# Kernel tuning notes

Measured on AMD Instinct MI355X. Metric: run time of the kernel, lower is better.

Reference implementation:

```python
import jax, jax.numpy as jnp
import numpy as np

NUM_DST = 100_000   # blk.num_dst()
E = 1_000_000       # number of temporal edges
U_N = 200_000       # unique node rows
U_E = 100_000       # unique edge-feature rows
U_T = 100_000       # unique time deltas
DN, DE, DT, DOUT, H = 172, 172, 100, 100, 2
NEG_SLOPE = 0.2
LN_EPS = 1e-5


def _lin_init(k, fan_in, fan_out):
    return jax.random.normal(k, (fan_in, fan_out), jnp.float32) / np.float32(np.sqrt(fan_in))


def setup_inputs() -> dict:
    key = jax.random.key(0)
    ks = jax.random.split(key, 16)
    return {
        "nodeData": jax.random.normal(ks[0], (U_N, DN), jnp.float32),
        "efeat_unique": jax.random.normal(ks[1], (U_E, DE), jnp.float32),
        "unique_time_delta": jax.random.uniform(ks[2], (U_T,), jnp.float32) * 1000.0,
        "reverse_nids": jax.random.randint(ks[3], (NUM_DST + E,), 0, U_N, jnp.int32),
        "reverse_eids": jax.random.randint(ks[4], (E,), 0, U_E, jnp.int32),
        "reverse_time_delta": jax.random.randint(ks[5], (E,), 0, U_T, jnp.int32),
        "dstindex": jax.random.randint(ks[6], (E,), 0, NUM_DST, jnp.int32),
        "num_dst": NUM_DST,
        "time_w": jax.random.normal(ks[7], (DT,), jnp.float32),
        "time_b": jax.random.normal(ks[8], (DT,), jnp.float32),
        "Wqn": _lin_init(ks[9], DN, DOUT), "bqn": jnp.zeros((DOUT,), jnp.float32),
        "Wqt": _lin_init(ks[10], DT, DOUT), "bqt": jnp.zeros((DOUT,), jnp.float32),
        "Wkvn": _lin_init(ks[11], DN, 2 * DOUT), "bkvn": jnp.zeros((2 * DOUT,), jnp.float32),
        "Wkve": _lin_init(ks[12], DE, 2 * DOUT), "bkve": jnp.zeros((2 * DOUT,), jnp.float32),
        "Wkvt": _lin_init(ks[13], DT, 2 * DOUT), "bkvt": jnp.zeros((2 * DOUT,), jnp.float32),
        "Wout": _lin_init(ks[14], DN + DOUT, DOUT), "bout": jnp.zeros((DOUT,), jnp.float32),
        "ln_g": jnp.ones((DOUT,), jnp.float32), "ln_b": jnp.zeros((DOUT,), jnp.float32),
    }


def _forward(nodeData, efeat_unique, unique_time_delta, time_w, time_b,
             Wqn, bqn, Wqt, bqt, Wkvn, bkvn, Wkve, bkve, Wkvt, bkvt,
             Wout, bout, ln_g, ln_b,
             reverse_nids, reverse_eids, reverse_time_delta, dstindex, num_dst):
    node_dst_inv = reverse_nids[:num_dst]   # dst -> unique node row
    node_inv = reverse_nids[num_dst:]       # edge -> unique node row (src/nbr)
    # TimeEncode: cos(t * w + b); t=0 for all dst nodes (single shared row).
    nbrs_time_feat = jnp.cos(unique_time_delta[:, None] * time_w[None, :] + time_b[None, :])  # [U_T, DT]
    time_dst = jnp.cos(time_b)[None, :]                                                       # [1, DT]
    # Queries: project unique tables once, then gather (dedup trick).
    q = (nodeData @ Wqn + bqn)[node_dst_inv] + (time_dst @ Wqt + bqt)  # [num_dst, DOUT]
    Q = q[dstindex]                                                    # [E, DOUT]
    # Keys/values: fused node+edge+time projections, gathered per edge.
    Z = ((nodeData @ Wkvn + bkvn)[node_inv]
         + (efeat_unique @ Wkve + bkve)[reverse_eids]
         + (nbrs_time_feat @ Wkvt + bkvt)[reverse_time_delta])         # [E, 2*DOUT]
    dh = DOUT // H
    K = Z[:, :DOUT].reshape(-1, H, dh)
    V = Z[:, DOUT:].reshape(-1, H, dh)
    Qh = Q.reshape(-1, H, dh)
    attn = jax.nn.leaky_relu(jnp.sum(Qh * K, axis=2), NEG_SLOPE)       # [E, H]
    # edge softmax over incoming edges of each dst node
    m = jax.lax.stop_gradient(jax.ops.segment_max(attn, dstindex, num_segments=num_dst))
    e = jnp.exp(attn - m[dstindex])
    s = jax.ops.segment_sum(e, dstindex, num_segments=num_dst)
    a = e / s[dstindex]                                                # [E, H]
    # edge reduce (sum) -> [num_dst, DOUT]
    out = jax.ops.segment_sum((V * a[:, :, None]).reshape(-1, DOUT), dstindex, num_segments=num_dst)
    out = jnp.concatenate([out, nodeData[node_dst_inv]], axis=1)       # [num_dst, DOUT+DN]
    out = jax.nn.relu(out @ Wout + bout)
    mu = out.mean(axis=-1, keepdims=True)
    var = out.var(axis=-1, keepdims=True)
    return (out - mu) / jnp.sqrt(var + LN_EPS) * ln_g + ln_b


def reference(nodeData, efeat_unique, unique_time_delta, reverse_nids, reverse_eids,
              reverse_time_delta, dstindex, num_dst, time_w, time_b,
              Wqn, bqn, Wqt, bqt, Wkvn, bkvn, Wkve, bkve, Wkvt, bkvt,
              Wout, bout, ln_g, ln_b):
    return _forward(nodeData, efeat_unique, unique_time_delta, time_w, time_b,
                    Wqn, bqn, Wqt, bqt, Wkvn, bkvn, Wkve, bkve, Wkvt, bkvt,
                    Wout, bout, ln_g, ln_b,
                    reverse_nids, reverse_eids, reverse_time_delta, dstindex, num_dst)
```

## Files before the change

### kernel.cpp

```cpp
#include <hip/hip_runtime.h>
#include <hip/hip_bf16.h>

typedef __hip_bfloat16 bf16;

#define K_NUM_DST 100000
#define K_E       1000000
#define K_UN      200000
#define K_UE      100000
#define K_UT      100000
#define K_DN      172
#define K_DT      100
#define K_DOUT    100
#define K_DKV     200
#define K_DCAT    272
#define K_NEG_SLOPE 0.2f
#define K_LN_EPS    1e-5f

__device__ __forceinline__ float bits2f(unsigned short u){
  union { float f; unsigned int i; } c; c.i = ((unsigned int)u) << 16; return c.f;
}
__device__ __forceinline__ float t2f(float v){ return v; }
__device__ __forceinline__ float t2f(bf16 v){ return __bfloat162float(v); }

template<typename TIN> struct OutStore;
template<> struct OutStore<float>{
  static __device__ __forceinline__ void st(void* o, size_t i, float v){ ((float*)o)[i] = v; }
};
template<> struct OutStore<bf16>{
  static __device__ __forceinline__ void st(void* o, size_t i, float v){ ((bf16*)o)[i] = __float2bfloat16(v); }
};

template<typename TIN> struct Ld4;
template<> struct Ld4<float>{
  static __device__ __forceinline__ float4 ld(const void* base, size_t eo){
    return *(const float4*)((const float*)base + eo);
  }
};
template<> struct Ld4<bf16>{
  static __device__ __forceinline__ float4 ld(const void* base, size_t eo){
    ushort4 u = *(const ushort4*)((const unsigned short*)base + eo);
    float4 f; f.x = bits2f(u.x); f.y = bits2f(u.y); f.z = bits2f(u.z); f.w = bits2f(u.w);
    return f;
  }
};

template<typename TAB> __device__ __forceinline__ void store4(TAB* p, float a, float b, float c, float d);
template<> __device__ __forceinline__ void store4<float>(float* p, float a, float b, float c, float d){
  float4 v; v.x=a; v.y=b; v.z=c; v.w=d; *(float4*)p = v;
}
template<> __device__ __forceinline__ void store4<bf16>(bf16* p, float a, float b, float c, float d){
  p[0]=__float2bfloat16(a); p[1]=__float2bfloat16(b); p[2]=__float2bfloat16(c); p[3]=__float2bfloat16(d);
}

__global__ void detect_kernel(const unsigned short* __restrict__ nd, int* __restrict__ dflag){
  unsigned int i = blockIdx.x * 256u + threadIdx.x;
  unsigned short u = nd[i];
  if (((u >> 7) & 0xFF) == 0xFF) atomicOr(dflag, 1);
}

template<typename TIN>
__global__ void qt_kernel(const int* __restrict__ dflag, int want,
                          const void* time_b_v, const void* Wqt_v,
                          const void* bqt_v, float* __restrict__ qt){
  if (*dflag != want) return;
  const TIN* time_b = (const TIN*)time_b_v;
  const TIN* Wqt = (const TIN*)Wqt_v;
  const TIN* bqt = (const TIN*)bqt_v;
  int c = threadIdx.x;
  if (c >= K_DOUT) return;
  float acc = t2f(bqt[c]);
  for (int k = 0; k < K_DT; k++)
    acc += cosf(t2f(time_b[k])) * t2f(Wqt[k * K_DOUT + c]);
  qt[c] = acc;
}

template<typename TAB, typename TIN>
__global__ __launch_bounds__(320)
void node_proj_kernel(const int* __restrict__ dflag, int want,
    const void* nodeData_v, const void* Wqn_v, const void* bqn_v,
    const void* Wkvn_v, const void* bkvn_v,
    TAB* __restrict__ qn_tab, TAB* __restrict__ kvn_tab){
  if (*dflag != want) return;
  __shared__ float xs[32][68];
  int row0 = blockIdx.x * 32;
  int tid = threadIdx.x;
  int ci = tid % 75, ri = tid / 75;
  const void* W; const TIN* B; int ldw, c0;
  if (ci < 25){ W = Wqn_v;  B = (const TIN*)bqn_v;  ldw = K_DOUT; c0 = 4*ci; }
  else        { W = Wkvn_v; B = (const TIN*)bkvn_v; ldw = K_DKV;  c0 = 4*(ci-25); }
  float acc[8][4] = {};
  #pragma unroll
  for (int c = 0; c < 3; c++){
    const int ng = (c < 2) ? 16 : 11;
    if (c > 0) __syncthreads();
    for (int idx = tid; idx < 32 * ng; idx += 320){
      int r = idx / ng, g = idx % ng;
      float4 v = Ld4<TIN>::ld(nodeData_v, (size_t)(row0 + r) * K_DN + (16*c + g) * 4);
      *(float4*)&xs[r][g * 4] = v;
    }
    __syncthreads();
    if (tid < 300){
      const float* xbase = &xs[8*ri][0];
      #pragma unroll 2
      for (int g = 0; g < ng; g++){
        int kg = (16*c + g) * 4;
        float4 w0 = Ld4<TIN>::ld(W, (size_t)(kg+0) * ldw + c0);
        float4 w1 = Ld4<TIN>::ld(W, (size_t)(kg+1) * ldw + c0);
        float4 w2 = Ld4<TIN>::ld(W, (size_t)(kg+2) * ldw + c0);
        float4 w3 = Ld4<TIN>::ld(W, (size_t)(kg+3) * ldw + c0);
        #pragma unroll
        for (int i = 0; i < 8; i++){
          float4 a = *(const float4*)(xbase + i * 68 + 4*g);
          acc[i][0] = fmaf(a.x,w0.x, fmaf(a.y,w1.x, fmaf(a.z,w2.x, fmaf(a.w,w3.x, acc[i][0]))));
          acc[i][1] = fmaf(a.x,w0.y, fmaf(a.y,w1.y, fmaf(a.z,w2.y, fmaf(a.w,w3.y, acc[i][1]))));
          acc[i][2] = fmaf(a.x,w0.z, fmaf(a.y,w1.z, fmaf(a.z,w2.z, fmaf(a.w,w3.z, acc[i][2]))));
          acc[i][3] = fmaf(a.x,w0.w, fmaf(a.y,w1.w, fmaf(a.z,w2.w, fmaf(a.w,w3.w, acc[i][3]))));
        }
      }
    }
  }
  if (tid >= 300) return;
  float b0 = t2f(B[c0+0]), b1 = t2f(B[c0+1]), b2 = t2f(B[c0+2]), b3 = t2f(B[c0+3]);
  TAB* tab = (ci < 25) ? qn_tab : kvn_tab;
  #pragma unroll
  for (int i = 0; i < 8; i++){
    size_t row = row0 + 8*ri + i;
    store4<TAB>(&tab[row * ldw + c0], acc[i][0]+b0, acc[i][1]+b1, acc[i][2]+b2, acc[i][3]+b3);
  }
}

template<typename TAB, typename TIN>
__global__ __launch_bounds__(256)
void feat_proj_kernel(const int* __restrict__ dflag, int want,
    const void* A_v, const void* W_v, const void* bias_v,
    TAB* __restrict__ out_tab){
  if (*dflag != want) return;
  __shared__ float xs[40][68];
  int row0 = blockIdx.x * 40;
  int tid = threadIdx.x;
  int ci = tid % 50, ri = tid / 50;
  int c0 = 4 * ci;
  float acc[8][4] = {};
  #pragma unroll
  for (int c = 0; c < 3; c++){
    const int ng = (c < 2) ? 16 : 11;
    if (c > 0) __syncthreads();
    for (int idx = tid; idx < 40 * ng; idx += 256){
      int r = idx / ng, g = idx % ng;
      float4 v = Ld4<TIN>::ld(A_v, (size_t)(row0 + r) * K_DN + (16*c + g) * 4);
      *(float4*)&xs[r][g * 4] = v;
    }
    __syncthreads();
    if (tid < 250){
      const float* xbase = &xs[8*ri][0];
      #pragma unroll 2
      for (int g = 0; g < ng; g++){
        int kg = (16*c + g) * 4;
        float4 w0 = Ld4<TIN>::ld(W_v, (size_t)(kg+0) * K_DKV + c0);
        float4 w1 = Ld4<TIN>::ld(W_v, (size_t)(kg+1) * K_DKV + c0);
        float4 w2 = Ld4<TIN>::ld(W_v, (size_t)(kg+2) * K_DKV + c0);
        float4 w3 = Ld4<TIN>::ld(W_v, (size_t)(kg+3) * K_DKV + c0);
        #pragma unroll
        for (int i = 0; i < 8; i++){
          float4 a = *(const float4*)(xbase + i * 68 + 4*g);
          acc[i][0] = fmaf(a.x,w0.x, fmaf(a.y,w1.x, fmaf(a.z,w2.x, fmaf(a.w,w3.x, acc[i][0]))));
          acc[i][1] = fmaf(a.x,w0.y, fmaf(a.y,w1.y, fmaf(a.z,w2.y, fmaf(a.w,w3.y, acc[i][1]))));
          acc[i][2] = fmaf(a.x,w0.z, fmaf(a.y,w1.z, fmaf(a.z,w2.z, fmaf(a.w,w3.z, acc[i][2]))));
          acc[i][3] = fmaf(a.x,w0.w, fmaf(a.y,w1.w, fmaf(a.z,w2.w, fmaf(a.w,w3.w, acc[i][3]))));
        }
      }
    }
  }
  if (tid >= 250) return;
  const TIN* B = (const TIN*)bias_v;
  float b0 = t2f(B[c0+0]), b1 = t2f(B[c0+1]), b2 = t2f(B[c0+2]), b3 = t2f(B[c0+3]);
  #pragma unroll
  for (int i = 0; i < 8; i++){
    size_t row = row0 + 8*ri + i;
    store4<TAB>(&out_tab[row * K_DKV + c0], acc[i][0]+b0, acc[i][1]+b1, acc[i][2]+b2, acc[i][3]+b3);
  }
}

template<typename TAB, typename TIN>
__global__ __launch_bounds__(256)
void time_proj_kernel(const int* __restrict__ dflag, int want,
    const void* utd_v, const void* time_w_v, const void* time_b_v,
    const void* Wkvt_v, const void* bkvt_v,
    TAB* __restrict__ kvt_tab){
  if (*dflag != want) return;
  __shared__ float xs[40][68];
  __shared__ float ts[40];
  int row0 = blockIdx.x * 40;
  int tid = threadIdx.x;
  if (tid < 40) ts[tid] = t2f(((const TIN*)utd_v)[row0 + tid]);
  __syncthreads();
  int ci = tid % 50, ri = tid / 50;
  int c0 = 4 * ci;
  float acc[8][4] = {};
  #pragma unroll
  for (int c = 0; c < 2; c++){
    const int ng = (c < 1) ? 16 : 9;
    const int nk = ng * 4;
    if (c > 0) __syncthreads();
    for (int idx = tid; idx < 40 * nk; idx += 256){
      int r = idx / nk, kloc = idx % nk;
      int k = 64*c + kloc;
      xs[r][kloc] = cosf(ts[r] * t2f(((const TIN*)time_w_v)[k]) + t2f(((const TIN*)time_b_v)[k]));
    }
    __syncthreads();
    if (tid < 250){
      const float* xbase = &xs[8*ri][0];
      #pragma unroll 2
      for (int g = 0; g < ng; g++){
        int kg = 64*c + 4*g;
        float4 w0 = Ld4<TIN>::ld(Wkvt_v, (size_t)(kg+0) * K_DKV + c0);
        float4 w1 = Ld4<TIN>::ld(Wkvt_v, (size_t)(kg+1) * K_DKV + c0);
        float4 w2 = Ld4<TIN>::ld(Wkvt_v, (size_t)(kg+2) * K_DKV + c0);
        float4 w3 = Ld4<TIN>::ld(Wkvt_v, (size_t)(kg+3) * K_DKV + c0);
        #pragma unroll
        for (int i = 0; i < 8; i++){
          float4 a = *(const float4*)(xbase + i * 68 + 4*g);
          acc[i][0] = fmaf(a.x,w0.x, fmaf(a.y,w1.x, fmaf(a.z,w2.x, fmaf(a.w,w3.x, acc[i][0]))));
          acc[i][1] = fmaf(a.x,w0.y, fmaf(a.y,w1.y, fmaf(a.z,w2.y, fmaf(a.w,w3.y, acc[i][1]))));
          acc[i][2] = fmaf(a.x,w0.z, fmaf(a.y,w1.z, fmaf(a.z,w2.z, fmaf(a.w,w3.z, acc[i][2]))));
          acc[i][3] = fmaf(a.x,w0.w, fmaf(a.y,w1.w, fmaf(a.z,w2.w, fmaf(a.w,w3.w, acc[i][3]))));
        }
      }
    }
  }
  if (tid >= 250) return;
  const TIN* B = (const TIN*)bkvt_v;
  float b0 = t2f(B[c0+0]), b1 = t2f(B[c0+1]), b2 = t2f(B[c0+2]), b3 = t2f(B[c0+3]);
  #pragma unroll
  for (int i = 0; i < 8; i++){
    size_t row = row0 + 8*ri + i;
    store4<TAB>(&kvt_tab[row * K_DKV + c0], acc[i][0]+b0, acc[i][1]+b1, acc[i][2]+b2, acc[i][3]+b3);
  }
}

__global__ void hist_kernel(const int* __restrict__ dstindex, int* __restrict__ counts){
  int e = blockIdx.x * blockDim.x + threadIdx.x;
  if (e < K_E) atomicAdd(&counts[dstindex[e]], 1);
}

__global__ void scan1_kernel(const int* __restrict__ counts, int* __restrict__ offsets,
                             int* __restrict__ bsum, int n){
  __shared__ int sd[256];
  int b = blockIdx.x, t = threadIdx.x;
  int base = b * 1024 + t * 4;
  int v0=0,v1=0,v2=0,v3=0;
  if (base+0 < n) v0 = counts[base+0];
  if (base+1 < n) v1 = counts[base+1];
  if (base+2 < n) v2 = counts[base+2];
  if (base+3 < n) v3 = counts[base+3];
  int s = v0+v1+v2+v3;
  sd[t] = s;
  __syncthreads();
  for (int off = 1; off < 256; off <<= 1){
    int tmp = (t >= off) ? sd[t-off] : 0;
    __syncthreads();
    sd[t] += tmp;
    __syncthreads();
  }
  int excl = sd[t] - s;
  if (base+0 < n) offsets[base+0] = excl;
  if (base+1 < n) offsets[base+1] = excl + v0;
  if (base+2 < n) offsets[base+2] = excl + v0 + v1;
  if (base+3 < n) offsets[base+3] = excl + v0 + v1 + v2;
  if (t == 255) bsum[b] = sd[255];
}

__global__ void scan2_kernel(int* bsum, int nb){
  if (threadIdx.x == 0 && blockIdx.x == 0){
    int run = 0;
    for (int i = 0; i < nb; i++){ int v = bsum[i]; bsum[i] = run; run += v; }
  }
}

__global__ void scan3_kernel(int* __restrict__ offsets, const int* __restrict__ bsum, int n){
  int i = blockIdx.x * blockDim.x + threadIdx.x;
  if (i < n) offsets[i] += bsum[i >> 10];
}

__global__ void scatter_kernel(const int* __restrict__ dstindex, const int* __restrict__ offsets,
                               int* __restrict__ cursor, int* __restrict__ edge_ids){
  int e = blockIdx.x * blockDim.x + threadIdx.x;
  if (e < K_E){
    int d = dstindex[e];
    int p = atomicAdd(&cursor[d], 1);
    edge_ids[offsets[d] + p] = e;
  }
}

template<typename TAB>
__global__ __launch_bounds__(256)
void attn_kernel(
    const int* __restrict__ reverse_nids, const int* __restrict__ reverse_eids,
    const int* __restrict__ reverse_tids,
    const int* __restrict__ dstoff, const int* __restrict__ dstcnt,
    const int* __restrict__ edge_ids,
    const TAB* __restrict__ qn_tab, const TAB* __restrict__ kvn_tab,
    const TAB* __restrict__ kve_tab, const TAB* __restrict__ kvt_tab,
    const float* __restrict__ qt, float* __restrict__ out_agg){
  int tid = threadIdx.x;
  int wave = tid >> 6;
  int l = tid & 63;
  int h = l >> 5;
  int li = l & 31;
  int dst = blockIdx.x * 4 + wave;
  int start = dstoff[dst];
  int cnt = dstcnt[dst];
  int cntw = (cnt + 1 - h) >> 1;
  bool act = (li < 25);
  int d4 = 4 * li;
  bool c0h0 = (d4+0) < 50, c1h0 = (d4+1) < 50, c2h0 = (d4+2) < 50, c3h0 = (d4+3) < 50;

  int gn = reverse_nids[dst];
  float4 q = make_float4(0.f,0.f,0.f,0.f);
  if (act){
    float4 qn = Ld4<TAB>::ld(qn_tab, (size_t)gn * K_DOUT + d4);
    float4 qtv = *(const float4*)(qt + d4);
    q.x = qn.x + qtv.x; q.y = qn.y + qtv.y; q.z = qn.z + qtv.z; q.w = qn.w + qtv.w;
  }

  float m0 = -3.0e38f, m1 = -3.0e38f, s0 = 0.f, s1 = 0.f;
  float ax = 0.f, ay = 0.f, az = 0.f, aw = 0.f;

  for (int j = 0; j < cntw; j++){
    int e   = edge_ids[start + 2*j + h];
    int nid = reverse_nids[K_NUM_DST + e];
    int eid = reverse_eids[e];
    int tde = reverse_tids[e];
    float4 kx = make_float4(0.f,0.f,0.f,0.f);
    if (act){
      float4 k1 = Ld4<TAB>::ld(kvn_tab, (size_t)nid * K_DKV + d4);
      float4 k2 = Ld4<TAB>::ld(kve_tab, (size_t)eid * K_DKV + d4);
      float4 k3 = Ld4<TAB>::ld(kvt_tab, (size_t)tde * K_DKV + d4);
      kx.x = k1.x+k2.x+k3.x; kx.y = k1.y+k2.y+k3.y; kx.z = k1.z+k2.z+k3.z; kx.w = k1.w+k2.w+k3.w;
    }
    float px = q.x*kx.x, py = q.y*kx.y, pz = q.z*kx.z, pw = q.w*kx.w;
    float p0 = (c0h0?px:0.f) + (c1h0?py:0.f) + (c2h0?pz:0.f) + (c3h0?pw:0.f);
    float p1 = (px+py+pz+pw) - p0;
    #pragma unroll
    for (int off = 16; off; off >>= 1){
      p0 += __shfl_xor(p0, off);
      p1 += __shfl_xor(p1, off);
    }
    float a0 = (p0 > 0.f) ? p0 : K_NEG_SLOPE * p0;
    float a1 = (p1 > 0.f) ? p1 : K_NEG_SLOPE * p1;
    float nm0 = fmaxf(m0, a0), nm1 = fmaxf(m1, a1);
    float al0 = __expf(m0 - nm0), al1 = __expf(m1 - nm1);
    float e0  = __expf(a0 - nm0), e1  = __expf(a1 - nm1);
    s0 = s0 * al0 + e0; s1 = s1 * al1 + e1;
    m0 = nm0; m1 = nm1;
    float4 vx = make_float4(0.f,0.f,0.f,0.f);
    if (act){
      float4 v1 = Ld4<TAB>::ld(kvn_tab, (size_t)nid * K_DKV + K_DOUT + d4);
      float4 v2 = Ld4<TAB>::ld(kve_tab, (size_t)eid * K_DKV + K_DOUT + d4);
      float4 v3 = Ld4<TAB>::ld(kvt_tab, (size_t)tde * K_DKV + K_DOUT + d4);
      vx.x = v1.x+v2.x+v3.x; vx.y = v1.y+v2.y+v3.y; vx.z = v1.z+v2.z+v3.z; vx.w = v1.w+v2.w+v3.w;
    }
    ax = ax * (c0h0?al0:al1) + (c0h0?e0:e1) * vx.x;
    ay = ay * (c1h0?al0:al1) + (c1h0?e0:e1) * vx.y;
    az = az * (c2h0?al0:al1) + (c2h0?e0:e1) * vx.z;
    aw = aw * (c3h0?al0:al1) + (c3h0?e0:e1) * vx.w;
  }

  float mo0 = __shfl_xor(m0, 32), so0 = __shfl_xor(s0, 32);
  float mo1 = __shfl_xor(m1, 32), so1 = __shfl_xor(s1, 32);
  float aox = __shfl_xor(ax, 32), aoy = __shfl_xor(ay, 32);
  float aoz = __shfl_xor(az, 32), aow = __shfl_xor(aw, 32);
  float M0 = fmaxf(m0, mo0), M1 = fmaxf(m1, mo1);
  float cs0 = __expf(m0 - M0), co0 = __expf(mo0 - M0);
  float cs1 = __expf(m1 - M1), co1 = __expf(mo1 - M1);
  float S0 = s0 * cs0 + so0 * co0;
  float S1 = s1 * cs1 + so1 * co1;
  float inv0 = (S0 > 0.f) ? 1.f / S0 : 0.f;
  float inv1 = (S1 > 0.f) ? 1.f / S1 : 0.f;
  float rx = c0h0 ? (ax*cs0 + aox*co0)*inv0 : (ax*cs1 + aox*co1)*inv1;
  float ry = c1h0 ? (ay*cs0 + aoy*co0)*inv0 : (ay*cs1 + aoy*co1)*inv1;
  float rz = c2h0 ? (az*cs0 + aoz*co0)*inv0 : (az*cs1 + aoz*co1)*inv1;
  float rw = c3h0 ? (aw*cs0 + aow*co0)*inv0 : (aw*cs1 + aow*co1)*inv1;
  if (h == 0 && act){
    float4 r; r.x=rx; r.y=ry; r.z=rz; r.w=rw;
    *(float4*)(out_agg + (size_t)dst * K_DOUT + d4) = r;
  }
}

template<typename TIN>
__global__ __launch_bounds__(256)
void final_kernel(const int* __restrict__ dflag, int want,
    const float* __restrict__ out_agg,
    const void* nodeData_v, const int* __restrict__ reverse_nids,
    const void* Wout_v, const void* bout_v,
    const void* ln_g_v, const void* ln_b_v,
    void* out){
  if (*dflag != want) return;
  __shared__ float xs[32][72];
  __shared__ float part[32][25][2];
  __shared__ float stats[32][2];
  __shared__ int gnid[32];
  int dbase = blockIdx.x * 32;
  int tid = threadIdx.x;
  if (tid < 32) gnid[tid] = reverse_nids[dbase + tid];
  __syncthreads();
  int ci = tid % 25, ri = tid / 25;
  int c0 = 4 * ci;
  float acc[4][4] = {};
  #pragma unroll
  for (int c = 0; c < 4; c++){
    if (c > 0) __syncthreads();
    for (int idx = tid; idx < 32 * 17; idx += 256){
      int r = idx / 17, g = idx % 17;
      int gk = (c * 17 + g) * 4;
      float4 v;
      if (gk < 100) v = *(const float4*)(out_agg + (size_t)(dbase + r) * K_DOUT + gk);
      else          v = Ld4<TIN>::ld(nodeData_v, (size_t)gnid[r] * K_DN + (gk - 100));
      *(float4*)&xs[r][g * 4] = v;
    }
    __syncthreads();
    if (tid < 200){
      const float* xbase = &xs[4 * ri][0];
      #pragma unroll 2
      for (int g = 0; g < 17; g++){
        int kg = (c * 17 + g) * 4;
        float4 w0 = Ld4<TIN>::ld(Wout_v, (size_t)(kg+0) * K_DOUT + c0);
        float4 w1 = Ld4<TIN>::ld(Wout_v, (size_t)(kg+1) * K_DOUT + c0);
        float4 w2 = Ld4<TIN>::ld(Wout_v, (size_t)(kg+2) * K_DOUT + c0);
        float4 w3 = Ld4<TIN>::ld(Wout_v, (size_t)(kg+3) * K_DOUT + c0);
        #pragma unroll
        for (int i = 0; i < 4; i++){
          float4 a = *(const float4*)(xbase + i * 72 + 4*g);
          acc[i][0] = fmaf(a.x,w0.x, fmaf(a.y,w1.x, fmaf(a.z,w2.x, fmaf(a.w,w3.x, acc[i][0]))));
          acc[i][1] = fmaf(a.x,w0.y, fmaf(a.y,w1.y, fmaf(a.z,w2.y, fmaf(a.w,w3.y, acc[i][1]))));
          acc[i][2] = fmaf(a.x,w0.z, fmaf(a.y,w1.z, fmaf(a.z,w2.z, fmaf(a.w,w3.z, acc[i][2]))));
          acc[i][3] = fmaf(a.x,w0.w, fmaf(a.y,w1.w, fmaf(a.z,w2.w, fmaf(a.w,w3.w, acc[i][3]))));
        }
      }
    }
  }
  if (tid < 200){
    const TIN* B = (const TIN*)bout_v;
    float b0 = t2f(B[c0+0]), b1 = t2f(B[c0+1]), b2 = t2f(B[c0+2]), b3 = t2f(B[c0+3]);
    #pragma unroll
    for (int i = 0; i < 4; i++){
      acc[i][0] = fmaxf(acc[i][0]+b0, 0.f);
      acc[i][1] = fmaxf(acc[i][1]+b1, 0.f);
      acc[i][2] = fmaxf(acc[i][2]+b2, 0.f);
      acc[i][3] = fmaxf(acc[i][3]+b3, 0.f);
      float s1 = acc[i][0]+acc[i][1]+acc[i][2]+acc[i][3];
      float s2 = acc[i][0]*acc[i][0]+acc[i][1]*acc[i][1]+acc[i][2]*acc[i][2]+acc[i][3]*acc[i][3];
      part[4*ri + i][ci][0] = s1;
      part[4*ri + i][ci][1] = s2;
    }
  }
  __syncthreads();
  if (tid < 32){
    float s1 = 0.f, s2 = 0.f;
    for (int j = 0; j < 25; j++){ s1 += part[tid][j][0]; s2 += part[tid][j][1]; }
    stats[tid][0] = s1; stats[tid][1] = s2;
  }
  __syncthreads();
  if (tid < 200){
    const TIN* G = (const TIN*)ln_g_v; const TIN* Bb = (const TIN*)ln_b_v;
    float g0 = t2f(G[c0+0]), g1 = t2f(G[c0+1]), g2 = t2f(G[c0+2]), g3 = t2f(G[c0+3]);
    float lb0 = t2f(Bb[c0+0]), lb1 = t2f(Bb[c0+1]), lb2 = t2f(Bb[c0+2]), lb3 = t2f(Bb[c0+3]);
    #pragma unroll
    for (int i = 0; i < 4; i++){
      int r = 4*ri + i;
      float mu = stats[r][0] * (1.f / K_DOUT);
      float var = stats[r][1] * (1.f / K_DOUT) - mu * mu;
      float rs = rsqrtf(var + K_LN_EPS);
      size_t o = (size_t)(dbase + r) * K_DOUT + c0;
      OutStore<TIN>::st(out, o+0, (acc[i][0]-mu)*rs*g0 + lb0);
      OutStore<TIN>::st(out, o+1, (acc[i][1]-mu)*rs*g1 + lb1);
      OutStore<TIN>::st(out, o+2, (acc[i][2]-mu)*rs*g2 + lb2);
      OutStore<TIN>::st(out, o+3, (acc[i][3]-mu)*rs*g3 + lb3);
    }
  }
}

static inline size_t al256(size_t b){ return (b + 255) & ~(size_t)255; }

template<typename TAB>
static void run_pipeline(void* const* d_in, void* out, char* ws, hipStream_t stream){
  const void* nodeData = d_in[0];
  const void* efeat    = d_in[1];
  const void* utd      = d_in[2];
  const int* reverse_nids = (const int*)d_in[3];
  const int* reverse_eids = (const int*)d_in[4];
  const int* reverse_tids = (const int*)d_in[5];
  const int* dstindex     = (const int*)d_in[6];
  const void* time_w = d_in[8];
  const void* time_b = d_in[9];
  const void* Wqn  = d_in[10]; const void* bqn  = d_in[11];
  const void* Wqt  = d_in[12]; const void* bqt  = d_in[13];
  const void* Wkvn = d_in[14]; const void* bkvn = d_in[15];
  const void* Wkve = d_in[16]; const void* bkve = d_in[17];
  const void* Wkvt = d_in[18]; const void* bkvt = d_in[19];
  const void* Wout = d_in[20]; const void* bout = d_in[21];
  const void* ln_g = d_in[22]; const void* ln_b = d_in[23];

  char* p = ws;
  int* dflag = (int*)p;       p += 256;
  TAB* qn_tab  = (TAB*)p; p += al256(sizeof(TAB) * (size_t)K_UN * K_DOUT);
  TAB* kvn_tab = (TAB*)p; p += al256(sizeof(TAB) * (size_t)K_UN * K_DKV);
  TAB* kve_tab = (TAB*)p; p += al256(sizeof(TAB) * (size_t)K_UE * K_DKV);
  TAB* kvt_tab = (TAB*)p; p += al256(sizeof(TAB) * (size_t)K_UT * K_DKV);
  float* out_agg = (float*)p; p += al256(sizeof(float) * (size_t)K_NUM_DST * K_DOUT);
  float* qt = (float*)p;      p += al256(sizeof(float) * K_DOUT);
  int* counts = (int*)p;      p += al256(sizeof(int) * K_NUM_DST);
  int* offsets = (int*)p;     p += al256(sizeof(int) * K_NUM_DST);
  int* cursor = (int*)p;      p += al256(sizeof(int) * K_NUM_DST);
  int* bsum = (int*)p;        p += al256(sizeof(int) * 512);
  int* edge_ids = (int*)p;    p += al256(sizeof(int) * (size_t)K_E);

  hipMemsetAsync(dflag, 0, 256, stream);
  hipMemsetAsync(counts, 0, sizeof(int) * K_NUM_DST, stream);
  hipMemsetAsync(cursor, 0, sizeof(int) * K_NUM_DST, stream);

  detect_kernel<<<512, 256, 0, stream>>>((const unsigned short*)nodeData, dflag);

  qt_kernel<float><<<1, 128, 0, stream>>>(dflag, 1, time_b, Wqt, bqt, qt);
  node_proj_kernel<TAB, float><<<K_UN / 32, 320, 0, stream>>>(dflag, 1, nodeData, Wqn, bqn, Wkvn, bkvn, qn_tab, kvn_tab);
  feat_proj_kernel<TAB, float><<<K_UE / 40, 256, 0, stream>>>(dflag, 1, efeat, Wkve, bkve, kve_tab);
  time_proj_kernel<TAB, float><<<K_UT / 40, 256, 0, stream>>>(dflag, 1, utd, time_w, time_b, Wkvt, bkvt, kvt_tab);
  qt_kernel<bf16><<<1, 128, 0, stream>>>(dflag, 0, time_b, Wqt, bqt, qt);
  node_proj_kernel<TAB, bf16><<<K_UN / 32, 320, 0, stream>>>(dflag, 0, nodeData, Wqn, bqn, Wkvn, bkvn, qn_tab, kvn_tab);
  feat_proj_kernel<TAB, bf16><<<K_UE / 40, 256, 0, stream>>>(dflag, 0, efeat, Wkve, bkve, kve_tab);
  time_proj_kernel<TAB, bf16><<<K_UT / 40, 256, 0, stream>>>(dflag, 0, utd, time_w, time_b, Wkvt, bkvt, kvt_tab);

  hist_kernel<<<(K_E + 255) / 256, 256, 0, stream>>>(dstindex, counts);
  int nb = (K_NUM_DST + 1023) / 1024;
  scan1_kernel<<<nb, 256, 0, stream>>>(counts, offsets, bsum, K_NUM_DST);
  scan2_kernel<<<1, 1, 0, stream>>>(bsum, nb);
  scan3_kernel<<<(K_NUM_DST + 255) / 256, 256, 0, stream>>>(offsets, bsum, K_NUM_DST);
  scatter_kernel<<<(K_E + 255) / 256, 256, 0, stream>>>(dstindex, offsets, cursor, edge_ids);

  attn_kernel<TAB><<<K_NUM_DST / 4, 256, 0, stream>>>(reverse_nids, reverse_eids, reverse_tids,
      offsets, counts, edge_ids, qn_tab, kvn_tab, kve_tab, kvt_tab, qt, out_agg);

  final_kernel<float><<<K_NUM_DST / 32, 256, 0, stream>>>(dflag, 1, out_agg, nodeData, reverse_nids,
      Wout, bout, ln_g, ln_b, out);
  final_kernel<bf16><<<K_NUM_DST / 32, 256, 0, stream>>>(dflag, 0, out_agg, nodeData, reverse_nids,
      Wout, bout, ln_g, ln_b, out);
}

extern "C" void kernel_launch(void* const* d_in, const int* in_sizes, int n_in,
                              void* d_out, int out_size, void* d_ws, size_t ws_size,
                              hipStream_t stream){
  (void)in_sizes; (void)n_in; (void)out_size;

  size_t fixed = 256 + al256(4ull * K_NUM_DST * K_DOUT) + al256(4 * K_DOUT)
               + 3 * al256(4 * K_NUM_DST) + al256(4 * 512) + al256(4ull * K_E);
  size_t tab_elems = (size_t)K_UN * K_DOUT + (size_t)K_UN * K_DKV
                   + (size_t)K_UE * K_DKV + (size_t)K_UT * K_DKV;
  size_t need_f32  = fixed + tab_elems * 4 + 8192;
  size_t need_bf16 = fixed + tab_elems * 2 + 8192;

  if (ws_size >= need_f32){
    run_pipeline<float>(d_in, d_out, (char*)d_ws, stream);
  } else if (ws_size >= need_bf16){
    run_pipeline<bf16>(d_in, d_out, (char*)d_ws, stream);
  }
}
```

Baseline: 1.738 ms.

## Use bf16 MFMA matrix cores for node, edge and time projection GEMMs

For bf16 inputs, the node, edge-feature and time projections move from scalar FMA kernels to MFMA 16x16x32 bf16 kernels. Small pre-pass kernels pack the weights into an MFMA-friendly fragment layout, and the time encoding is computed into shared memory before the matmul. The aim is to cut projection compute time. The cost is extra launches, extra workspace, and bf16 rounding of the cos time features.

```diff
diff --git a/kernel.cpp b/kernel.cpp
--- a/kernel.cpp
+++ b/kernel.cpp
@@ -2,6 +2,9 @@
 #include <hip/hip_bf16.h>
 
 typedef __hip_bfloat16 bf16;
+typedef unsigned short u16;
+typedef __attribute__((ext_vector_type(8))) short bf16x8s;
+typedef __attribute__((ext_vector_type(4))) float f32x4;
 
 #define K_NUM_DST 100000
 #define K_E       1000000
@@ -16,8 +19,21 @@
 #define K_NEG_SLOPE 0.2f
 #define K_LN_EPS    1e-5f
 
-__device__ __forceinline__ float bits2f(unsigned short u){
+#define NT_NODE 19
+#define NS_NODE 6
+#define NT_KV   13
+#define NS_KVE  6
+#define NS_KVT  4
+
+__device__ __forceinline__ float bits2f(u16 u){
   union { float f; unsigned int i; } c; c.i = ((unsigned int)u) << 16; return c.f;
+}
+__device__ __forceinline__ u16 f2bfbits(float f){
+  bf16 h = __float2bfloat16(f);
+  return *(u16*)&h;
+}
+__device__ __forceinline__ unsigned int pk2(float a, float b){
+  return (unsigned int)f2bfbits(a) | ((unsigned int)f2bfbits(b) << 16);
 }
 __device__ __forceinline__ float t2f(float v){ return v; }
 __device__ __forceinline__ float t2f(bf16 v){ return __bfloat162float(v); }
@@ -38,7 +54,7 @@
 };
 template<> struct Ld4<bf16>{
   static __device__ __forceinline__ float4 ld(const void* base, size_t eo){
-    ushort4 u = *(const ushort4*)((const unsigned short*)base + eo);
+    ushort4 u = *(const ushort4*)((const u16*)base + eo);
     float4 f; f.x = bits2f(u.x); f.y = bits2f(u.y); f.z = bits2f(u.z); f.w = bits2f(u.w);
     return f;
   }
@@ -52,9 +68,9 @@
   p[0]=__float2bfloat16(a); p[1]=__float2bfloat16(b); p[2]=__float2bfloat16(c); p[3]=__float2bfloat16(d);
 }
 
-__global__ void detect_kernel(const unsigned short* __restrict__ nd, int* __restrict__ dflag){
+__global__ void detect_kernel(const u16* __restrict__ nd, int* __restrict__ dflag){
   unsigned int i = blockIdx.x * 256u + threadIdx.x;
-  unsigned short u = nd[i];
+  u16 u = nd[i];
   if (((u >> 7) & 0xFF) == 0xFF) atomicOr(dflag, 1);
 }
 
@@ -72,6 +88,166 @@
   for (int k = 0; k < K_DT; k++)
     acc += cosf(t2f(time_b[k])) * t2f(Wqt[k * K_DOUT + c]);
   qt[c] = acc;
+}
+
+
+__global__ void pack_node_w_kernel(const int* __restrict__ dflag,
+    const u16* __restrict__ Wqn, const u16* __restrict__ Wkvn, u16* __restrict__ Bp){
+  if (*dflag != 0) return;
+  int t = blockIdx.x * 256 + threadIdx.x;
+  if (t >= NT_NODE * NS_NODE * 64) return;
+  int lane = t & 63; int cs = t >> 6; int s = cs % NS_NODE, c = cs / NS_NODE;
+  int col = c * 16 + (lane & 15);
+  int k0 = s * 32 + (lane >> 4) * 8;
+  u16 v[8];
+  #pragma unroll
+  for (int e = 0; e < 8; e++){
+    int k = k0 + e; u16 x = 0;
+    if (k < K_DN){
+      if (col < K_DOUT) x = Wqn[(size_t)k * K_DOUT + col];
+      else if (col < K_DOUT + K_DKV) x = Wkvn[(size_t)k * K_DKV + (col - K_DOUT)];
+    }
+    v[e] = x;
+  }
+  uint4 o;
+  o.x = (unsigned)v[0] | ((unsigned)v[1] << 16);
+  o.y = (unsigned)v[2] | ((unsigned)v[3] << 16);
+  o.z = (unsigned)v[4] | ((unsigned)v[5] << 16);
+  o.w = (unsigned)v[6] | ((unsigned)v[7] << 16);
+  *(uint4*)&Bp[(size_t)t * 8] = o;
+}
+
+__global__ void pack_w_kernel(const int* __restrict__ dflag,
+    const u16* __restrict__ W, int K, int N, int NT, int NS, u16* __restrict__ Bp){
+  if (*dflag != 0) return;
+  int t = blockIdx.x * 256 + threadIdx.x;
+  if (t >= NT * NS * 64) return;
+  int lane = t & 63; int cs = t >> 6; int s = cs % NS, c = cs / NS;
+  int col = c * 16 + (lane & 15);
+  int k0 = s * 32 + (lane >> 4) * 8;
+  u16 v[8];
+  #pragma unroll
+  for (int e = 0; e < 8; e++){
+    int k = k0 + e;
+    v[e] = (k < K && col < N) ? W[(size_t)k * N + col] : (u16)0;
+  }
+  uint4 o;
+  o.x = (unsigned)v[0] | ((unsigned)v[1] << 16);
+  o.y = (unsigned)v[2] | ((unsigned)v[3] << 16);
+  o.z = (unsigned)v[4] | ((unsigned)v[5] << 16);
+  o.w = (unsigned)v[6] | ((unsigned)v[7] << 16);
+  *(uint4*)&Bp[(size_t)t * 8] = o;
+}
+
+template<typename TAB>
+__global__ __launch_bounds__(256)
+void mfma_proj_kernel(const int* __restrict__ dflag,
+    const u16* __restrict__ A, int M,
+    const u16* __restrict__ Bp, int NT,
+    const u16* __restrict__ bias1, const u16* __restrict__ bias2,
+    TAB* __restrict__ out1, int N1, TAB* __restrict__ out2, int N2){
+  if (*dflag != 0) return;
+  __shared__ u16 xs[64][200];
+  int row0 = blockIdx.x * 64;
+  int tid = threadIdx.x;
+  const unsigned int* A32 = (const unsigned int*)A;
+  unsigned int* xs32 = (unsigned int*)&xs[0][0];
+  for (int j = tid; j < 64 * 86; j += 256){
+    int r = j / 86, k2 = j % 86;
+    unsigned int v = (row0 + r < M) ? A32[(size_t)(row0 + r) * 86 + k2] : 0u;
+    xs32[r * 100 + k2] = v;
+  }
+  for (int j = tid; j < 64 * 14; j += 256){
+    int r = j / 14, k2 = 86 + (j % 14);
+    xs32[r * 100 + k2] = 0u;
+  }
+  __syncthreads();
+  int lane = tid & 63, w = tid >> 6;
+  int ar = 16 * w + (lane & 15);
+  int kg = lane >> 4;
+  bf16x8s a[6];
+  #pragma unroll
+  for (int s = 0; s < 6; s++)
+    a[s] = *(const bf16x8s*)&xs[ar][s * 32 + kg * 8];
+  int co_l = lane & 15;
+  int rb = row0 + 16 * w + 4 * kg;
+  for (int c = 0; c < NT; c++){
+    const u16* bp = Bp + (size_t)(c * 6) * 512 + (size_t)lane * 8;
+    f32x4 acc = {0.f, 0.f, 0.f, 0.f};
+    #pragma unroll
+    for (int s = 0; s < 6; s++){
+      bf16x8s b = *(const bf16x8s*)(bp + s * 512);
+      acc = __builtin_amdgcn_mfma_f32_16x16x32_bf16(a[s], b, acc, 0, 0, 0);
+    }
+    int co = c * 16 + co_l;
+    float bv; TAB* op; size_t stride; int cc;
+    if (co < N1){ bv = bits2f(bias1[co]); op = out1; stride = N1; cc = co; }
+    else if (co < N1 + N2){ bv = bits2f(bias2[co - N1]); op = out2; stride = N2; cc = co - N1; }
+    else continue;
+    #pragma unroll
+    for (int r = 0; r < 4; r++){
+      int row = rb + r;
+      if (row < M) OutStore<TAB>::st(op, (size_t)row * stride + cc, acc[r] + bv);
+    }
+  }
+}
+
+template<typename TAB>
+__global__ __launch_bounds__(256)
+void mfma_time_proj_kernel(const int* __restrict__ dflag,
+    const u16* __restrict__ utd, int M,
+    const u16* __restrict__ Bp,
+    const u16* __restrict__ tw, const u16* __restrict__ tb,
+    const u16* __restrict__ bias, TAB* __restrict__ out1){
+  if (*dflag != 0) return;
+  __shared__ u16 xs[64][136];
+  __shared__ float ts[64];
+  int row0 = blockIdx.x * 64;
+  int tid = threadIdx.x;
+  if (tid < 64){
+    int r = row0 + tid;
+    ts[tid] = bits2f(utd[(r < M) ? r : (M - 1)]);
+  }
+  __syncthreads();
+  unsigned int* xs32 = (unsigned int*)&xs[0][0];
+  for (int j = tid; j < 64 * 68; j += 256){
+    int r = j / 68, k2 = j % 68;
+    int k = k2 * 2;
+    unsigned int v = 0u;
+    if (k < K_DT){
+      float c0 = cosf(ts[r] * bits2f(tw[k])     + bits2f(tb[k]));
+      float c1 = cosf(ts[r] * bits2f(tw[k + 1]) + bits2f(tb[k + 1]));
+      v = pk2(c0, c1);
+    }
+    xs32[r * 68 + k2] = v;
+  }
+  __syncthreads();
+  int lane = tid & 63, w = tid >> 6;
+  int ar = 16 * w + (lane & 15);
+  int kg = lane >> 4;
+  bf16x8s a[4];
+  #pragma unroll
+  for (int s = 0; s < 4; s++)
+    a[s] = *(const bf16x8s*)&xs[ar][s * 32 + kg * 8];
+  int co_l = lane & 15;
+  int rb = row0 + 16 * w + 4 * kg;
+  for (int c = 0; c < NT_KV; c++){
+    const u16* bp = Bp + (size_t)(c * 4) * 512 + (size_t)lane * 8;
+    f32x4 acc = {0.f, 0.f, 0.f, 0.f};
+    #pragma unroll
+    for (int s = 0; s < 4; s++){
+      bf16x8s b = *(const bf16x8s*)(bp + s * 512);
+      acc = __builtin_amdgcn_mfma_f32_16x16x32_bf16(a[s], b, acc, 0, 0, 0);
+    }
+    int co = c * 16 + co_l;
+    if (co >= K_DKV) continue;
+    float bv = bits2f(bias[co]);
+    #pragma unroll
+    for (int r = 0; r < 4; r++){
+      int row = rb + r;
+      if (row < M) OutStore<TAB>::st(out1, (size_t)row * K_DKV + co, acc[r] + bv);
+    }
+  }
 }
 
 template<typename TAB, typename TIN>
@@ -482,6 +658,10 @@
 
 static inline size_t al256(size_t b){ return (b + 255) & ~(size_t)255; }
 
+#define BP_NODE_U16 ((size_t)NT_NODE * NS_NODE * 64 * 8)
+#define BP_KVE_U16  ((size_t)NT_KV * NS_KVE * 64 * 8)
+#define BP_KVT_U16  ((size_t)NT_KV * NS_KVT * 64 * 8)
+
 template<typename TAB>
 static void run_pipeline(void* const* d_in, void* out, char* ws, hipStream_t stream){
   const void* nodeData = d_in[0];
@@ -514,21 +694,37 @@
   int* cursor = (int*)p;      p += al256(sizeof(int) * K_NUM_DST);
   int* bsum = (int*)p;        p += al256(sizeof(int) * 512);
   int* edge_ids = (int*)p;    p += al256(sizeof(int) * (size_t)K_E);
+  u16* bp_node = (u16*)p;     p += al256(2 * BP_NODE_U16);
+  u16* bp_kve  = (u16*)p;     p += al256(2 * BP_KVE_U16);
+  u16* bp_kvt  = (u16*)p;     p += al256(2 * BP_KVT_U16);
 
   hipMemsetAsync(dflag, 0, 256, stream);
   hipMemsetAsync(counts, 0, sizeof(int) * K_NUM_DST, stream);
   hipMemsetAsync(cursor, 0, sizeof(int) * K_NUM_DST, stream);
 
-  detect_kernel<<<512, 256, 0, stream>>>((const unsigned short*)nodeData, dflag);
+  detect_kernel<<<512, 256, 0, stream>>>((const u16*)nodeData, dflag);
 
   qt_kernel<float><<<1, 128, 0, stream>>>(dflag, 1, time_b, Wqt, bqt, qt);
   node_proj_kernel<TAB, float><<<K_UN / 32, 320, 0, stream>>>(dflag, 1, nodeData, Wqn, bqn, Wkvn, bkvn, qn_tab, kvn_tab);
   feat_proj_kernel<TAB, float><<<K_UE / 40, 256, 0, stream>>>(dflag, 1, efeat, Wkve, bkve, kve_tab);
   time_proj_kernel<TAB, float><<<K_UT / 40, 256, 0, stream>>>(dflag, 1, utd, time_w, time_b, Wkvt, bkvt, kvt_tab);
+
   qt_kernel<bf16><<<1, 128, 0, stream>>>(dflag, 0, time_b, Wqt, bqt, qt);
-  node_proj_kernel<TAB, bf16><<<K_UN / 32, 320, 0, stream>>>(dflag, 0, nodeData, Wqn, bqn, Wkvn, bkvn, qn_tab, kvn_tab);
-  feat_proj_kernel<TAB, bf16><<<K_UE / 40, 256, 0, stream>>>(dflag, 0, efeat, Wkve, bkve, kve_tab);
-  time_proj_kernel<TAB, bf16><<<K_UT / 40, 256, 0, stream>>>(dflag, 0, utd, time_w, time_b, Wkvt, bkvt, kvt_tab);
+  pack_node_w_kernel<<<(NT_NODE*NS_NODE*64 + 255)/256, 256, 0, stream>>>(
+      dflag, (const u16*)Wqn, (const u16*)Wkvn, bp_node);
+  pack_w_kernel<<<(NT_KV*NS_KVE*64 + 255)/256, 256, 0, stream>>>(
+      dflag, (const u16*)Wkve, K_DN, K_DKV, NT_KV, NS_KVE, bp_kve);
+  pack_w_kernel<<<(NT_KV*NS_KVT*64 + 255)/256, 256, 0, stream>>>(
+      dflag, (const u16*)Wkvt, K_DT, K_DKV, NT_KV, NS_KVT, bp_kvt);
+  mfma_proj_kernel<TAB><<<K_UN / 64, 256, 0, stream>>>(
+      dflag, (const u16*)nodeData, K_UN, bp_node, NT_NODE,
+      (const u16*)bqn, (const u16*)bkvn, qn_tab, K_DOUT, kvn_tab, K_DKV);
+  mfma_proj_kernel<TAB><<<(K_UE + 63) / 64, 256, 0, stream>>>(
+      dflag, (const u16*)efeat, K_UE, bp_kve, NT_KV,
+      (const u16*)bkve, (const u16*)bkve, kve_tab, K_DKV, (TAB*)nullptr, 0);
+  mfma_time_proj_kernel<TAB><<<(K_UT + 63) / 64, 256, 0, stream>>>(
+      dflag, (const u16*)utd, K_UT, bp_kvt,
+      (const u16*)time_w, (const u16*)time_b, (const u16*)bkvt, kvt_tab);
 
   hist_kernel<<<(K_E + 255) / 256, 256, 0, stream>>>(dstindex, counts);
   int nb = (K_NUM_DST + 1023) / 1024;
@@ -552,7 +748,8 @@
   (void)in_sizes; (void)n_in; (void)out_size;
 
   size_t fixed = 256 + al256(4ull * K_NUM_DST * K_DOUT) + al256(4 * K_DOUT)
-               + 3 * al256(4 * K_NUM_DST) + al256(4 * 512) + al256(4ull * K_E);
+               + 3 * al256(4 * K_NUM_DST) + al256(4 * 512) + al256(4ull * K_E)
+               + al256(2 * BP_NODE_U16) + al256(2 * BP_KVE_U16) + al256(2 * BP_KVT_U16);
   size_t tab_elems = (size_t)K_UN * K_DOUT + (size_t)K_UN * K_DKV
                    + (size_t)K_UE * K_DKV + (size_t)K_UT * K_DKV;
   size_t need_f32  = fixed + tab_elems * 4 + 8192;
```

Measured after the change: 1.737 ms. About the same (-0.0%).
